# Performance work log

Measured on AMD Instinct MI355X. Metric: run time of the kernel, lower is better.

## Reference

```python
import math
import jax, jax.numpy as jnp
import numpy as np

D_MODEL = 2048
HEAD = 128
DEPTH = 12
LAMBDA_INIT = 0.8 - 0.6 * math.exp(-0.3 * DEPTH)
RMS_EPS = float(np.finfo(np.float32).eps)  # torch RMSNorm default eps=None -> finfo.eps


def setup_inputs() -> dict:
    key = jax.random.key(0)
    ks = jax.random.split(key, 9)
    B, S = 2, 4096
    std_l = 0.1
    return {
        "x": jax.random.normal(ks[0], (B, S, D_MODEL), dtype=jnp.float32),
        "Wq": jax.random.normal(ks[1], (HEAD, D_MODEL), dtype=jnp.float32) / math.sqrt(D_MODEL),
        "Wk": jax.random.normal(ks[2], (HEAD, D_MODEL), dtype=jnp.float32) / math.sqrt(D_MODEL),
        "Wv": jax.random.normal(ks[3], (HEAD, D_MODEL), dtype=jnp.float32) / math.sqrt(D_MODEL),
        "lambda_q1": std_l * jax.random.normal(ks[4], (HEAD // 2,), dtype=jnp.float32),
        "lambda_q2": std_l * jax.random.normal(ks[5], (HEAD // 2,), dtype=jnp.float32),
        "lambda_k1": std_l * jax.random.normal(ks[6], (HEAD // 2,), dtype=jnp.float32),
        "lambda_k2": std_l * jax.random.normal(ks[7], (HEAD // 2,), dtype=jnp.float32),
        "rms_weight": jnp.ones((HEAD,), dtype=jnp.float32),
    }


def reference(x, Wq, Wk, Wv, lambda_q1, lambda_q2, lambda_k1, lambda_k2, rms_weight):
    # projections (torch Linear: x @ W.T)
    q = jnp.einsum("bsd,hd->bsh", x, Wq)
    k = jnp.einsum("bsd,hd->bsh", x, Wk)
    v = jnp.einsum("bsd,hd->bsh", x, Wv)
    h2 = HEAD // 2
    q1, q2 = q[..., :h2], q[..., h2:]
    k1, k2 = k[..., :h2], k[..., h2:]
    scale = 1.0 / math.sqrt(h2)
    attn1 = jax.nn.softmax(jnp.einsum("bqh,bkh->bqk", q1, k1) * scale, axis=-1)
    attn2 = jax.nn.softmax(jnp.einsum("bqh,bkh->bqk", q2, k2) * scale, axis=-1)
    lam = jnp.exp(jnp.dot(lambda_q1, lambda_k1)) - jnp.exp(jnp.dot(lambda_q2, lambda_k2)) + LAMBDA_INIT
    attn_out = jnp.einsum("bqk,bkh->bqh", attn1 - lam * attn2, v)
    # RMSNorm over last dim
    rms = jax.lax.rsqrt(jnp.mean(attn_out * attn_out, axis=-1, keepdims=True) + RMS_EPS)
    return (1.0 - LAMBDA_INIT) * (attn_out * rms * rms_weight)
```

## Files before the change

kernel.cpp:

```cpp
#include <hip/hip_runtime.h>
#include <hip/hip_bf16.h>
#include <math.h>

#define S_LEN 4096
#define DMODEL 2048
#define HEADD 128

typedef __attribute__((ext_vector_type(8))) short short8;
typedef __attribute__((ext_vector_type(4))) float floatx4;

__device__ __forceinline__ short f2bs(float f) {
  __hip_bfloat16 h = __float2bfloat16(f);
  short s; __builtin_memcpy(&s, &h, 2); return s;
}
__device__ __forceinline__ float bs2f(short s) {
  unsigned u = ((unsigned)(unsigned short)s) << 16;
  float f; __builtin_memcpy(&f, &u, 4); return f;
}
__device__ __forceinline__ int pkbf(float a, float b) {
  return (int)(((unsigned)(unsigned short)f2bs(b) << 16) |
               (unsigned)(unsigned short)f2bs(a));
}

__global__ __launch_bounds__(256) void convw_kernel(const float* __restrict__ wq,
                                                    const float* __restrict__ wk,
                                                    const float* __restrict__ wv,
                                                    short* __restrict__ wc) {
  const int per = 128 * 2048;
  int e = (blockIdx.x * blockDim.x + threadIdx.x) * 4;
  const float* src = (e < per) ? wq : (e < 2 * per) ? wk : wv;
  int off = e & (per - 1);
  float4 v = *(const float4*)(src + off);
  short4 r;
  r.x = f2bs(v.x); r.y = f2bs(v.y); r.z = f2bs(v.z); r.w = f2bs(v.w);
  *(short4*)(wc + e) = r;
}

__global__ __launch_bounds__(256, 4) void proj_kernel(const float* __restrict__ x,
                                                      const short* __restrict__ wc,
                                                      short* __restrict__ qm,
                                                      short* __restrict__ kb,
                                                      short* __restrict__ vstage) {
  const int tid = threadIdx.x;
  const int w = tid >> 6;
  const int lane = tid & 63;
  const int lo = lane & 15, g = lane >> 4;
  const int id = blockIdx.x;
  const int nq = id >> 8, mb = id & 255;
  const int m0 = mb * 32;
  const int n0 = nq * 96;

  __shared__ short xt[2][16 * 64];
  __shared__ short wt[2][48 * 64];

  const int xr = tid >> 2, xc = tid & 3;
  const bool doX = tid < 128;
  const float* xsrc = x + (size_t)(m0 + (doX ? xr : 0)) * DMODEL + xc * 8;
  const int xl = (xr >> 1) * 64 + ((((xr & 1) * 4 + xc) ^ ((xr >> 1) & 7)) * 8);

  const int wr = tid >> 2, wq = tid & 3;
  const bool doW2 = tid < 128;
  const short* wsrc = wc + (size_t)(n0 + wr) * DMODEL + wq * 8;
  const short* wsrc2 = wc + (size_t)(n0 + wr + 64) * DMODEL + wq * 8;
  int wl1, wl2;
  {
    int R1 = wr, R2 = wr + 64;
    wl1 = (R1 >> 1) * 64 + ((((R1 & 1) * 4 + wq) ^ ((R1 >> 1) & 7)) * 8);
    wl2 = (R2 >> 1) * 64 + ((((R2 & 1) * 4 + wq) ^ ((R2 >> 1) & 7)) * 8);
  }

  const int mrow = (w >> 1) * 16;
  const int ncol = (w & 1) * 48;
  int aoff;
  { int r = mrow + lo; aoff = (r >> 1) * 64 + ((((r & 1) * 4 + g) ^ ((r >> 1) & 7)) * 8); }
  int boff[3];
#pragma unroll
  for (int t = 0; t < 3; ++t) {
    int R = ncol + t * 16 + lo;
    boff[t] = (R >> 1) * 64 + ((((R & 1) * 4 + g) ^ ((R >> 1) & 7)) * 8);
  }

  floatx4 acc[3];
#pragma unroll
  for (int t = 0; t < 3; ++t) acc[t] = floatx4{0.f, 0.f, 0.f, 0.f};

  float4 xa0, xa1, xb0, xb1;
  int4 wa1, wa2, wb1, wb2;

  if (doX) { xa0 = *(const float4*)(xsrc); xa1 = *(const float4*)(xsrc + 4); }
  wa1 = *(const int4*)(wsrc);
  if (doW2) wa2 = *(const int4*)(wsrc2);
  if (doX) {
    short8 xs;
    xs[0] = f2bs(xa0.x); xs[1] = f2bs(xa0.y); xs[2] = f2bs(xa0.z); xs[3] = f2bs(xa0.w);
    xs[4] = f2bs(xa1.x); xs[5] = f2bs(xa1.y); xs[6] = f2bs(xa1.z); xs[7] = f2bs(xa1.w);
    *(short8*)&xt[0][xl] = xs;
  }
  *(int4*)&wt[0][wl1] = wa1;
  if (doW2) *(int4*)&wt[0][wl2] = wa2;
  if (doX) { xb0 = *(const float4*)(xsrc + 32); xb1 = *(const float4*)(xsrc + 36); }
  wb1 = *(const int4*)(wsrc + 32);
  if (doW2) wb2 = *(const int4*)(wsrc2 + 32);
  __syncthreads();

#pragma unroll 1
  for (int it = 0; it < 64; it += 2) {
    if (it + 2 < 64) {
      const int k = (it + 2) * 32;
      if (doX) { xa0 = *(const float4*)(xsrc + k); xa1 = *(const float4*)(xsrc + k + 4); }
      wa1 = *(const int4*)(wsrc + k);
      if (doW2) wa2 = *(const int4*)(wsrc2 + k);
    }
    {
      short8 af = *(const short8*)&xt[0][aoff];
#pragma unroll
      for (int t = 0; t < 3; ++t) {
        short8 bf = *(const short8*)&wt[0][boff[t]];
        acc[t] = __builtin_amdgcn_mfma_f32_16x16x32_bf16(af, bf, acc[t], 0, 0, 0);
      }
    }
    if (doX) {
      short8 xs;
      xs[0] = f2bs(xb0.x); xs[1] = f2bs(xb0.y); xs[2] = f2bs(xb0.z); xs[3] = f2bs(xb0.w);
      xs[4] = f2bs(xb1.x); xs[5] = f2bs(xb1.y); xs[6] = f2bs(xb1.z); xs[7] = f2bs(xb1.w);
      *(short8*)&xt[1][xl] = xs;
    }
    *(int4*)&wt[1][wl1] = wb1;
    if (doW2) *(int4*)&wt[1][wl2] = wb2;
    __syncthreads();

    if (it + 3 < 64) {
      const int k = (it + 3) * 32;
      if (doX) { xb0 = *(const float4*)(xsrc + k); xb1 = *(const float4*)(xsrc + k + 4); }
      wb1 = *(const int4*)(wsrc + k);
      if (doW2) wb2 = *(const int4*)(wsrc2 + k);
    }
    {
      short8 af = *(const short8*)&xt[1][aoff];
#pragma unroll
      for (int t = 0; t < 3; ++t) {
        short8 bf = *(const short8*)&wt[1][boff[t]];
        acc[t] = __builtin_amdgcn_mfma_f32_16x16x32_bf16(af, bf, acc[t], 0, 0, 0);
      }
    }
    if (it + 2 < 64) {
      if (doX) {
        short8 xs;
        xs[0] = f2bs(xa0.x); xs[1] = f2bs(xa0.y); xs[2] = f2bs(xa0.z); xs[3] = f2bs(xa0.w);
        xs[4] = f2bs(xa1.x); xs[5] = f2bs(xa1.y); xs[6] = f2bs(xa1.z); xs[7] = f2bs(xa1.w);
        *(short8*)&xt[0][xl] = xs;
      }
      *(int4*)&wt[0][wl1] = wa1;
      if (doW2) *(int4*)&wt[0][wl2] = wa2;
    }
    __syncthreads();
  }

#pragma unroll
  for (int t = 0; t < 3; ++t) {
    int n = n0 + ncol + t * 16 + lo;
#pragma unroll
    for (int j = 0; j < 4; ++j) {
      int m = m0 + mrow + g * 4 + j;
      float v = acc[t][j];
      if (n < HEADD) {
        qm[(size_t)m * HEADD + n] = f2bs(v * 0.125f);
      } else if (n < 2 * HEADD) {
        kb[(size_t)m * HEADD + (n - HEADD)] = f2bs(v);
      } else {
        vstage[(size_t)m * HEADD + (n - 2 * HEADD)] = f2bs(v);
      }
    }
  }
}

__global__ __launch_bounds__(256) void conv_v_kernel(const short* __restrict__ vstage,
                                                     short* __restrict__ vt) {
  const int tid = threadIdx.x;
  const int bb = blockIdx.x >> 6, st = blockIdx.x & 63;
  const int s0 = st * 64;

  __shared__ short ld[64][136];

  const int r = tid >> 2, c8 = (tid & 3) * 32;
#pragma unroll
  for (int q = 0; q < 4; ++q) {
    const size_t off = (size_t)(bb * 4096 + s0 + r) * 128 + c8 + q * 8;
    *(short8*)(&ld[r][c8 + q * 8]) = *(const short8*)(vstage + off);
  }
  __syncthreads();

  const int h = tid >> 1, sh = (tid & 1) * 32;
#pragma unroll
  for (int q = 0; q < 4; ++q) {
    short8 t;
#pragma unroll
    for (int i = 0; i < 8; ++i) t[i] = ld[sh + q * 8 + i][h];
    *(short8*)(vt + ((size_t)bb * 128 + h) * 4096 + s0 + sh + q * 8) = t;
  }
}

__global__ __launch_bounds__(256, 3) void attn_kernel(const short* __restrict__ qm,
                                                      const short* __restrict__ kb,
                                                      const short* __restrict__ vt,
                                                      short* __restrict__ po,
                                                      float* __restrict__ pls) {
  const int tid = threadIdx.x;
  const int w = tid >> 6;
  const int lane = tid & 63;
  const int lo = lane & 15, g = lane >> 4;
  const int qsp = w >> 1;
  const int s = w & 1;
  const int id = blockIdx.x;
  const int ksp = id & 7;
  const int qblk = id >> 3;
  const int b = qblk >> 6;
  const int kv_base = ksp * 512;

  __shared__ short kt[2][32 * 128];
  __shared__ short vl[2][128 * 32];

  const int kr0 = tid >> 4, kck = tid & 15;
  const int vr0 = tid >> 2, vck = tid & 3;
  const short* kS = kb + (size_t)b * S_LEN * HEADD;
  const short* vS = vt + (size_t)b * HEADD * S_LEN;
  const int kld0 = kr0 * 128 + ((kck ^ (kr0 & 7)) * 8);
  const int kld1 = (kr0 + 16) * 128 + ((kck ^ (kr0 & 7)) * 8);
  const int vld0 = vr0 * 32 + ((vck ^ (vr0 & 3)) * 8);
  const int vld1 = (vr0 + 64) * 32 + ((vck ^ (vr0 & 3)) * 8);

  const int rowqA = qblk * 64 + qsp * 32;
  const int rowqB = rowqA + 16;
  const short* qrowA = qm + (size_t)(rowqA + lo) * HEADD + s * 64;
  const short* qrowB = qm + (size_t)(rowqB + lo) * HEADD + s * 64;
  const short8 qA0 = *(const short8*)(qrowA + g * 8);
  const short8 qA1 = *(const short8*)(qrowA + 32 + g * 8);
  const short8 qB0 = *(const short8*)(qrowB + g * 8);
  const short8 qB1 = *(const short8*)(qrowB + 32 + g * 8);

  floatx4 accA[8], accB[8];
#pragma unroll
  for (int n = 0; n < 8; ++n) {
    accA[n] = floatx4{0.f, 0.f, 0.f, 0.f};
    accB[n] = floatx4{0.f, 0.f, 0.f, 0.f};
  }
  float lxA = 0.f, lxB = 0.f;

  const int kc0 = ((s * 8 + g) ^ (lo & 7)) * 8;
  const int kc1 = ((s * 8 + 4 + g) ^ (lo & 7)) * 8;
  const int kro0 = lo * 128, kro1 = (16 + lo) * 128;
  const int vco = (g ^ (lo & 3)) * 8;

  const int gA = (g & 1) * 2;
  const int idx0 = lo + 16 * gA, idx1 = idx0 + 16;
  const bool hi = (g >= 2);

  {
    int4 ka = *(const int4*)(kS + (size_t)(kv_base + kr0) * HEADD + kck * 8);
    int4 kbx = *(const int4*)(kS + (size_t)(kv_base + kr0 + 16) * HEADD + kck * 8);
    int4 va = *(const int4*)(vS + (size_t)vr0 * S_LEN + kv_base + vck * 8);
    int4 vb = *(const int4*)(vS + (size_t)(vr0 + 64) * S_LEN + kv_base + vck * 8);
    *(int4*)(&kt[0][kld0]) = ka;
    *(int4*)(&kt[0][kld1]) = kbx;
    *(int4*)(&vl[0][vld0]) = va;
    *(int4*)(&vl[0][vld1]) = vb;
  }
  __syncthreads();

  int cur = 0;
#pragma unroll 1
  for (int it = 0; it < 16; ++it) {
    int4 ka, kbx, va, vb;
    if (it + 1 < 16) {
      const int kvn = kv_base + (it + 1) * 32;
      ka  = *(const int4*)(kS + (size_t)(kvn + kr0) * HEADD + kck * 8);
      kbx = *(const int4*)(kS + (size_t)(kvn + kr0 + 16) * HEADD + kck * 8);
      va  = *(const int4*)(vS + (size_t)vr0 * S_LEN + kvn + vck * 8);
      vb  = *(const int4*)(vS + (size_t)(vr0 + 64) * S_LEN + kvn + vck * 8);
    }

    const short* kbase = &kt[cur][0];
    short8 a00 = *(const short8*)(kbase + kro0 + kc0);
    short8 a01 = *(const short8*)(kbase + kro0 + kc1);
    short8 a10 = *(const short8*)(kbase + kro1 + kc0);
    short8 a11 = *(const short8*)(kbase + kro1 + kc1);

    floatx4 z = floatx4{0.f, 0.f, 0.f, 0.f};
    floatx4 u;
    u = __builtin_amdgcn_mfma_f32_16x16x32_bf16(a00, qA0, z, 0, 0, 0);
    floatx4 T0A = __builtin_amdgcn_mfma_f32_16x16x32_bf16(a01, qA1, u, 0, 0, 0);
    u = __builtin_amdgcn_mfma_f32_16x16x32_bf16(a10, qA0, z, 0, 0, 0);
    floatx4 T1A = __builtin_amdgcn_mfma_f32_16x16x32_bf16(a11, qA1, u, 0, 0, 0);
    u = __builtin_amdgcn_mfma_f32_16x16x32_bf16(a00, qB0, z, 0, 0, 0);
    floatx4 T0B = __builtin_amdgcn_mfma_f32_16x16x32_bf16(a01, qB1, u, 0, 0, 0);
    u = __builtin_amdgcn_mfma_f32_16x16x32_bf16(a10, qB0, z, 0, 0, 0);
    floatx4 T1B = __builtin_amdgcn_mfma_f32_16x16x32_bf16(a11, qB1, u, 0, 0, 0);

    short8 paA, paB;
    {
      float p0 = __expf(T0A[0]), p1 = __expf(T0A[1]), p2 = __expf(T0A[2]), p3 = __expf(T0A[3]);
      float p4 = __expf(T1A[0]), p5 = __expf(T1A[1]), p6 = __expf(T1A[2]), p7 = __expf(T1A[3]);
      float lp = ((p0 + p1) + (p2 + p3)) + ((p4 + p5) + (p6 + p7));
      lp += __shfl_xor(lp, 16);
      lp += __shfl_xor(lp, 32);
      lxA += lp;
      int c00 = pkbf(p0, p1), c01 = pkbf(p2, p3);
      int c10 = pkbf(p4, p5), c11 = pkbf(p6, p7);
      int t0a = __shfl(c00, idx0), t0b = __shfl(c01, idx0);
      int t0c = __shfl(c00, idx1), t0d = __shfl(c01, idx1);
      int t1a = __shfl(c10, idx0), t1b = __shfl(c11, idx0);
      int t1c = __shfl(c10, idx1), t1d = __shfl(c11, idx1);
      int w0 = hi ? t1a : t0a, w1 = hi ? t1b : t0b;
      int w2 = hi ? t1c : t0c, w3 = hi ? t1d : t0d;
      int4 tmp = {w0, w1, w2, w3}; __builtin_memcpy(&paA, &tmp, 16);
    }
    {
      float p0 = __expf(T0B[0]), p1 = __expf(T0B[1]), p2 = __expf(T0B[2]), p3 = __expf(T0B[3]);
      float p4 = __expf(T1B[0]), p5 = __expf(T1B[1]), p6 = __expf(T1B[2]), p7 = __expf(T1B[3]);
      float lp = ((p0 + p1) + (p2 + p3)) + ((p4 + p5) + (p6 + p7));
      lp += __shfl_xor(lp, 16);
      lp += __shfl_xor(lp, 32);
      lxB += lp;
      int c00 = pkbf(p0, p1), c01 = pkbf(p2, p3);
      int c10 = pkbf(p4, p5), c11 = pkbf(p6, p7);
      int t0a = __shfl(c00, idx0), t0b = __shfl(c01, idx0);
      int t0c = __shfl(c00, idx1), t0d = __shfl(c01, idx1);
      int t1a = __shfl(c10, idx0), t1b = __shfl(c11, idx0);
      int t1c = __shfl(c10, idx1), t1d = __shfl(c11, idx1);
      int w0 = hi ? t1a : t0a, w1 = hi ? t1b : t0b;
      int w2 = hi ? t1c : t0c, w3 = hi ? t1d : t0d;
      int4 tmp = {w0, w1, w2, w3}; __builtin_memcpy(&paB, &tmp, 16);
    }

    const short* vbase = &vl[cur][0];
#pragma unroll
    for (int n = 0; n < 8; ++n) {
      short8 vf = *(const short8*)(vbase + (n * 16 + lo) * 32 + vco);
      accA[n] = __builtin_amdgcn_mfma_f32_16x16x32_bf16(paA, vf, accA[n], 0, 0, 0);
      accB[n] = __builtin_amdgcn_mfma_f32_16x16x32_bf16(paB, vf, accB[n], 0, 0, 0);
    }

    if (it + 1 < 16) {
      *(int4*)(&kt[cur ^ 1][kld0]) = ka;
      *(int4*)(&kt[cur ^ 1][kld1]) = kbx;
      *(int4*)(&vl[cur ^ 1][vld0]) = va;
      *(int4*)(&vl[cur ^ 1][vld1]) = vb;
    }
    __syncthreads();
    cur ^= 1;
  }

  short* pw = po + ((size_t)(ksp * 2 + s) * 8192) * 128;
#pragma unroll
  for (int j = 0; j < 4; ++j) {
    short8 pk;
#pragma unroll
    for (int n = 0; n < 8; ++n) pk[n] = f2bs(accA[n][j]);
    *(short8*)(pw + (size_t)(rowqA + g * 4 + j) * 128 + lo * 8) = pk;
#pragma unroll
    for (int n = 0; n < 8; ++n) pk[n] = f2bs(accB[n][j]);
    *(short8*)(pw + (size_t)(rowqB + g * 4 + j) * 128 + lo * 8) = pk;
  }
  if (g == 0) {
    pls[(size_t)(ksp * 2 + s) * 8192 + rowqA + lo] = lxA;
    pls[(size_t)(ksp * 2 + s) * 8192 + rowqB + lo] = lxB;
  }
}

__global__ __launch_bounds__(256) void merge_kernel(const short* __restrict__ po,
                                                    const float* __restrict__ pls,
                                                    const float* __restrict__ lq1,
                                                    const float* __restrict__ lq2,
                                                    const float* __restrict__ lk1,
                                                    const float* __restrict__ lk2,
                                                    const float* __restrict__ rmsw,
                                                    float* __restrict__ out) {
  const int tid = threadIdx.x;
  const int row = blockIdx.x * 16 + (tid >> 4);
  const int lo = tid & 15;

  float a1s = 0.f, a2s = 0.f;
  for (int i = 0; i < 64; ++i) {
    a1s = fmaf(lq1[i], lk1[i], a1s);
    a2s = fmaf(lq2[i], lk2[i], a2s);
  }
  const float lam = __expf(a1s) - __expf(a2s) + 0.7836057665316245f;

  float o1[8], o2[8];
#pragma unroll
  for (int n = 0; n < 8; ++n) { o1[n] = 0.f; o2[n] = 0.f; }
  float l1 = 0.f, l2 = 0.f;
#pragma unroll
  for (int ksp = 0; ksp < 8; ++ksp) {
    short8 sa = *(const short8*)(po + ((size_t)(ksp * 2 + 0) * 8192 + row) * 128 + lo * 8);
    short8 sb = *(const short8*)(po + ((size_t)(ksp * 2 + 1) * 8192 + row) * 128 + lo * 8);
#pragma unroll
    for (int n = 0; n < 8; ++n) { o1[n] += bs2f(sa[n]); o2[n] += bs2f(sb[n]); }
    l1 += pls[(size_t)(ksp * 2 + 0) * 8192 + row];
    l2 += pls[(size_t)(ksp * 2 + 1) * 8192 + row];
  }
  const float iL1 = 1.f / l1, iL2 = 1.f / l2;

  float v[8];
  float ssq = 0.f;
#pragma unroll
  for (int n = 0; n < 8; ++n) {
    v[n] = o1[n] * iL1 - lam * (o2[n] * iL2);
    ssq += v[n] * v[n];
  }
  ssq += __shfl_xor(ssq, 1);
  ssq += __shfl_xor(ssq, 2);
  ssq += __shfl_xor(ssq, 4);
  ssq += __shfl_xor(ssq, 8);
  const float rr = rsqrtf(ssq * (1.f / 128.f) + 1.1920928955078125e-07f);

  float* ob = out + (size_t)row * 128;
#pragma unroll
  for (int n = 0; n < 8; ++n) {
    int c = n * 16 + lo;
    ob[c] = 0.21639423346837554f * v[n] * rr * rmsw[c];
  }
}

extern "C" void kernel_launch(void* const* d_in, const int* in_sizes, int n_in,
                              void* d_out, int out_size, void* d_ws, size_t ws_size,
                              hipStream_t stream) {
  const float* x   = (const float*)d_in[0];
  const float* wq  = (const float*)d_in[1];
  const float* wk  = (const float*)d_in[2];
  const float* wv  = (const float*)d_in[3];
  const float* lq1 = (const float*)d_in[4];
  const float* lq2 = (const float*)d_in[5];
  const float* lk1 = (const float*)d_in[6];
  const float* lk2 = (const float*)d_in[7];
  const float* rw  = (const float*)d_in[8];
  float* out = (float*)d_out;

  char* ws = (char*)d_ws;
  short* qm  = (short*)(ws);
  short* kb  = (short*)(ws + (2u << 20));
  short* vt  = (short*)(ws + (4u << 20));
  short* wc  = (short*)(ws + (6u << 20));
  short* vstage = (short*)(ws + (6u << 20) + 1572864u);
  short* po  = (short*)(ws + (8u << 20));
  float* pls = (float*)(ws + (40u << 20));

  convw_kernel<<<768, 256, 0, stream>>>(wq, wk, wv, wc);
  proj_kernel<<<1024, 256, 0, stream>>>(x, wc, qm, kb, vstage);
  conv_v_kernel<<<128, 256, 0, stream>>>(vstage, vt);
  attn_kernel<<<1024, 256, 0, stream>>>(qm, kb, vt, po, pls);
  merge_kernel<<<512, 256, 0, stream>>>(po, pls, lq1, lq2, lk1, lk2, rw, out);
}
```

Baseline: 104.6 us.

## Enlarge projection GEMM tile to 64 rows and 64-wide K steps

The projection kernel now computes a 64x96 output tile per block instead of 32x96, with each wave doing a 2x3 grid of MFMA tiles over a 64-wide K chunk per stage. This halves the grid to 512 blocks and the number of K-loop iterations and barriers, and improves reuse of each loaded W and x fragment. In exchange it uses more LDS and registers, so the occupancy hint drops from 4 to 3 blocks per CU. Fewer blocks may also leave some CUs idle.

After: 97.16 us. 7.1% less time.

```diff
diff --git a/kernel.cpp b/kernel.cpp
--- a/kernel.cpp
+++ b/kernel.cpp
@@ -36,7 +36,7 @@
   *(short4*)(wc + e) = r;
 }
 
-__global__ __launch_bounds__(256, 4) void proj_kernel(const float* __restrict__ x,
+__global__ __launch_bounds__(256, 3) void proj_kernel(const float* __restrict__ x,
                                                       const short* __restrict__ wc,
                                                       short* __restrict__ qm,
                                                       short* __restrict__ kb,
@@ -46,131 +46,136 @@
   const int lane = tid & 63;
   const int lo = lane & 15, g = lane >> 4;
   const int id = blockIdx.x;
-  const int nq = id >> 8, mb = id & 255;
-  const int m0 = mb * 32;
+  const int nq = id >> 7, mb = id & 127;
+  const int m0 = mb * 64;
   const int n0 = nq * 96;
 
-  __shared__ short xt[2][16 * 64];
-  __shared__ short wt[2][48 * 64];
-
-  const int xr = tid >> 2, xc = tid & 3;
-  const bool doX = tid < 128;
-  const float* xsrc = x + (size_t)(m0 + (doX ? xr : 0)) * DMODEL + xc * 8;
-  const int xl = (xr >> 1) * 64 + ((((xr & 1) * 4 + xc) ^ ((xr >> 1) & 7)) * 8);
-
-  const int wr = tid >> 2, wq = tid & 3;
-  const bool doW2 = tid < 128;
-  const short* wsrc = wc + (size_t)(n0 + wr) * DMODEL + wq * 8;
-  const short* wsrc2 = wc + (size_t)(n0 + wr + 64) * DMODEL + wq * 8;
-  int wl1, wl2;
+  __shared__ short xt[2][64 * 64];
+  __shared__ short wt[2][96 * 64];
+
+  const int r8 = tid >> 3, sc = tid & 7;
+  const float* xs0 = x + (size_t)(m0 + r8) * DMODEL + sc * 8;
+  const float* xs1 = x + (size_t)(m0 + 32 + r8) * DMODEL + sc * 8;
+  const short* ws0 = wc + (size_t)(n0 + r8) * DMODEL + sc * 8;
+  const short* ws1 = wc + (size_t)(n0 + 32 + r8) * DMODEL + sc * 8;
+  const short* ws2 = wc + (size_t)(n0 + 64 + r8) * DMODEL + sc * 8;
+  const int xl0 = r8 * 64 + ((sc ^ (r8 & 7)) * 8);
+  const int xl1 = (32 + r8) * 64 + ((sc ^ (r8 & 7)) * 8);
+  const int wlo0 = r8 * 64 + ((sc ^ (r8 & 7)) * 8);
+  const int wlo1 = (32 + r8) * 64 + ((sc ^ (r8 & 7)) * 8);
+  const int wlo2 = (64 + r8) * 64 + ((sc ^ (r8 & 7)) * 8);
+
+  const int mrow = (w >> 1) * 32;
+  const int ncol = (w & 1) * 48;
+  int aoff[2][2], boff[3][2];
+#pragma unroll
+  for (int mi = 0; mi < 2; ++mi) {
+    int r = mrow + mi * 16 + lo;
+#pragma unroll
+    for (int kc = 0; kc < 2; ++kc)
+      aoff[mi][kc] = r * 64 + (((kc * 4 + g) ^ (r & 7)) * 8);
+  }
+#pragma unroll
+  for (int t = 0; t < 3; ++t) {
+    int r = ncol + t * 16 + lo;
+#pragma unroll
+    for (int kc = 0; kc < 2; ++kc)
+      boff[t][kc] = r * 64 + (((kc * 4 + g) ^ (r & 7)) * 8);
+  }
+
+  floatx4 acc[2][3];
+#pragma unroll
+  for (int mi = 0; mi < 2; ++mi)
+#pragma unroll
+    for (int t = 0; t < 3; ++t) acc[mi][t] = floatx4{0.f, 0.f, 0.f, 0.f};
+
   {
-    int R1 = wr, R2 = wr + 64;
-    wl1 = (R1 >> 1) * 64 + ((((R1 & 1) * 4 + wq) ^ ((R1 >> 1) & 7)) * 8);
-    wl2 = (R2 >> 1) * 64 + ((((R2 & 1) * 4 + wq) ^ ((R2 >> 1) & 7)) * 8);
-  }
-
-  const int mrow = (w >> 1) * 16;
-  const int ncol = (w & 1) * 48;
-  int aoff;
-  { int r = mrow + lo; aoff = (r >> 1) * 64 + ((((r & 1) * 4 + g) ^ ((r >> 1) & 7)) * 8); }
-  int boff[3];
-#pragma unroll
-  for (int t = 0; t < 3; ++t) {
-    int R = ncol + t * 16 + lo;
-    boff[t] = (R >> 1) * 64 + ((((R & 1) * 4 + g) ^ ((R >> 1) & 7)) * 8);
-  }
-
-  floatx4 acc[3];
-#pragma unroll
-  for (int t = 0; t < 3; ++t) acc[t] = floatx4{0.f, 0.f, 0.f, 0.f};
-
-  float4 xa0, xa1, xb0, xb1;
-  int4 wa1, wa2, wb1, wb2;
-
-  if (doX) { xa0 = *(const float4*)(xsrc); xa1 = *(const float4*)(xsrc + 4); }
-  wa1 = *(const int4*)(wsrc);
-  if (doW2) wa2 = *(const int4*)(wsrc2);
-  if (doX) {
-    short8 xs;
-    xs[0] = f2bs(xa0.x); xs[1] = f2bs(xa0.y); xs[2] = f2bs(xa0.z); xs[3] = f2bs(xa0.w);
-    xs[4] = f2bs(xa1.x); xs[5] = f2bs(xa1.y); xs[6] = f2bs(xa1.z); xs[7] = f2bs(xa1.w);
-    *(short8*)&xt[0][xl] = xs;
-  }
-  *(int4*)&wt[0][wl1] = wa1;
-  if (doW2) *(int4*)&wt[0][wl2] = wa2;
-  if (doX) { xb0 = *(const float4*)(xsrc + 32); xb1 = *(const float4*)(xsrc + 36); }
-  wb1 = *(const int4*)(wsrc + 32);
-  if (doW2) wb2 = *(const int4*)(wsrc2 + 32);
+    float4 a0 = *(const float4*)(xs0), a1 = *(const float4*)(xs0 + 4);
+    float4 b0 = *(const float4*)(xs1), b1 = *(const float4*)(xs1 + 4);
+    int4 w0 = *(const int4*)(ws0);
+    int4 w1 = *(const int4*)(ws1);
+    int4 w2 = *(const int4*)(ws2);
+    short8 sA, sB;
+    sA[0]=f2bs(a0.x); sA[1]=f2bs(a0.y); sA[2]=f2bs(a0.z); sA[3]=f2bs(a0.w);
+    sA[4]=f2bs(a1.x); sA[5]=f2bs(a1.y); sA[6]=f2bs(a1.z); sA[7]=f2bs(a1.w);
+    sB[0]=f2bs(b0.x); sB[1]=f2bs(b0.y); sB[2]=f2bs(b0.z); sB[3]=f2bs(b0.w);
+    sB[4]=f2bs(b1.x); sB[5]=f2bs(b1.y); sB[6]=f2bs(b1.z); sB[7]=f2bs(b1.w);
+    *(short8*)&xt[0][xl0] = sA;
+    *(short8*)&xt[0][xl1] = sB;
+    *(int4*)&wt[0][wlo0] = w0;
+    *(int4*)&wt[0][wlo1] = w1;
+    *(int4*)&wt[0][wlo2] = w2;
+  }
   __syncthreads();
 
+  int cur = 0;
 #pragma unroll 1
-  for (int it = 0; it < 64; it += 2) {
-    if (it + 2 < 64) {
-      const int k = (it + 2) * 32;
-      if (doX) { xa0 = *(const float4*)(xsrc + k); xa1 = *(const float4*)(xsrc + k + 4); }
-      wa1 = *(const int4*)(wsrc + k);
-      if (doW2) wa2 = *(const int4*)(wsrc2 + k);
-    }
+  for (int it = 0; it < 32; ++it) {
+    float4 a0, a1, b0, b1;
+    int4 w0, w1, w2;
+    if (it + 1 < 32) {
+      const int k = (it + 1) * 64;
+      a0 = *(const float4*)(xs0 + k); a1 = *(const float4*)(xs0 + k + 4);
+      b0 = *(const float4*)(xs1 + k); b1 = *(const float4*)(xs1 + k + 4);
+      w0 = *(const int4*)(ws0 + k);
+      w1 = *(const int4*)(ws1 + k);
+      w2 = *(const int4*)(ws2 + k);
+    }
+
     {
-      short8 af = *(const short8*)&xt[0][aoff];
-#pragma unroll
-      for (int t = 0; t < 3; ++t) {
-        short8 bf = *(const short8*)&wt[0][boff[t]];
-        acc[t] = __builtin_amdgcn_mfma_f32_16x16x32_bf16(af, bf, acc[t], 0, 0, 0);
-      }
-    }
-    if (doX) {
-      short8 xs;
-      xs[0] = f2bs(xb0.x); xs[1] = f2bs(xb0.y); xs[2] = f2bs(xb0.z); xs[3] = f2bs(xb0.w);
-      xs[4] = f2bs(xb1.x); xs[5] = f2bs(xb1.y); xs[6] = f2bs(xb1.z); xs[7] = f2bs(xb1.w);
-      *(short8*)&xt[1][xl] = xs;
-    }
-    *(int4*)&wt[1][wl1] = wb1;
-    if (doW2) *(int4*)&wt[1][wl2] = wb2;
+      const short* xb = &xt[cur][0];
+      const short* wb = &wt[cur][0];
+      short8 af[2][2], bf[3][2];
+#pragma unroll
+      for (int mi = 0; mi < 2; ++mi)
+#pragma unroll
+        for (int kc = 0; kc < 2; ++kc) af[mi][kc] = *(const short8*)(xb + aoff[mi][kc]);
+#pragma unroll
+      for (int t = 0; t < 3; ++t)
+#pragma unroll
+        for (int kc = 0; kc < 2; ++kc) bf[t][kc] = *(const short8*)(wb + boff[t][kc]);
+#pragma unroll
+      for (int kc = 0; kc < 2; ++kc)
+#pragma unroll
+        for (int mi = 0; mi < 2; ++mi)
+#pragma unroll
+          for (int t = 0; t < 3; ++t)
+            acc[mi][t] = __builtin_amdgcn_mfma_f32_16x16x32_bf16(af[mi][kc], bf[t][kc], acc[mi][t], 0, 0, 0);
+    }
+
+    if (it + 1 < 32) {
+      short8 sA, sB;
+      sA[0]=f2bs(a0.x); sA[1]=f2bs(a0.y); sA[2]=f2bs(a0.z); sA[3]=f2bs(a0.w);
+      sA[4]=f2bs(a1.x); sA[5]=f2bs(a1.y); sA[6]=f2bs(a1.z); sA[7]=f2bs(a1.w);
+      sB[0]=f2bs(b0.x); sB[1]=f2bs(b0.y); sB[2]=f2bs(b0.z); sB[3]=f2bs(b0.w);
+      sB[4]=f2bs(b1.x); sB[5]=f2bs(b1.y); sB[6]=f2bs(b1.z); sB[7]=f2bs(b1.w);
+      *(short8*)&xt[cur ^ 1][xl0] = sA;
+      *(short8*)&xt[cur ^ 1][xl1] = sB;
+      *(int4*)&wt[cur ^ 1][wlo0] = w0;
+      *(int4*)&wt[cur ^ 1][wlo1] = w1;
+      *(int4*)&wt[cur ^ 1][wlo2] = w2;
+    }
     __syncthreads();
-
-    if (it + 3 < 64) {
-      const int k = (it + 3) * 32;
-      if (doX) { xb0 = *(const float4*)(xsrc + k); xb1 = *(const float4*)(xsrc + k + 4); }
-      wb1 = *(const int4*)(wsrc + k);
-      if (doW2) wb2 = *(const int4*)(wsrc2 + k);
-    }
-    {
-      short8 af = *(const short8*)&xt[1][aoff];
-#pragma unroll
-      for (int t = 0; t < 3; ++t) {
-        short8 bf = *(const short8*)&wt[1][boff[t]];
-        acc[t] = __builtin_amdgcn_mfma_f32_16x16x32_bf16(af, bf, acc[t], 0, 0, 0);
-      }
-    }
-    if (it + 2 < 64) {
-      if (doX) {
-        short8 xs;
-        xs[0] = f2bs(xa0.x); xs[1] = f2bs(xa0.y); xs[2] = f2bs(xa0.z); xs[3] = f2bs(xa0.w);
-        xs[4] = f2bs(xa1.x); xs[5] = f2bs(xa1.y); xs[6] = f2bs(xa1.z); xs[7] = f2bs(xa1.w);
-        *(short8*)&xt[0][xl] = xs;
-      }
-      *(int4*)&wt[0][wl1] = wa1;
-      if (doW2) *(int4*)&wt[0][wl2] = wa2;
-    }
-    __syncthreads();
+    cur ^= 1;
   }
 
 #pragma unroll
   for (int t = 0; t < 3; ++t) {
     int n = n0 + ncol + t * 16 + lo;
 #pragma unroll
-    for (int j = 0; j < 4; ++j) {
-      int m = m0 + mrow + g * 4 + j;
-      float v = acc[t][j];
-      if (n < HEADD) {
-        qm[(size_t)m * HEADD + n] = f2bs(v * 0.125f);
-      } else if (n < 2 * HEADD) {
-        kb[(size_t)m * HEADD + (n - HEADD)] = f2bs(v);
-      } else {
-        vstage[(size_t)m * HEADD + (n - 2 * HEADD)] = f2bs(v);
+    for (int mi = 0; mi < 2; ++mi)
+#pragma unroll
+      for (int j = 0; j < 4; ++j) {
+        int m = m0 + mrow + mi * 16 + g * 4 + j;
+        float v = acc[mi][t][j];
+        if (n < HEADD) {
+          qm[(size_t)m * HEADD + n] = f2bs(v * 0.125f);
+        } else if (n < 2 * HEADD) {
+          kb[(size_t)m * HEADD + (n - HEADD)] = f2bs(v);
+        } else {
+          vstage[(size_t)m * HEADD + (n - 2 * HEADD)] = f2bs(v);
+        }
       }
-    }
   }
 }
 
@@ -446,7 +451,7 @@
   float* pls = (float*)(ws + (40u << 20));
 
   convw_kernel<<<768, 256, 0, stream>>>(wq, wk, wv, wc);
-  proj_kernel<<<1024, 256, 0, stream>>>(x, wc, qm, kb, vstage);
+  proj_kernel<<<512, 256, 0, stream>>>(x, wc, qm, kb, vstage);
   conv_v_kernel<<<128, 256, 0, stream>>>(vstage, vt);
   attn_kernel<<<1024, 256, 0, stream>>>(qm, kb, vt, po, pls);
   merge_kernel<<<512, 256, 0, stream>>>(po, pls, lq1, lq2, lk1, lk2, rw, out);
```
